# Performance work log

Measured on AMD Instinct MI355X. Metric: run time of the kernel, lower is better.

## Reference

```python
import jax, jax.numpy as jnp
import numpy as np

HIDDEN = 1024
HEADS = 16
HEAD_DIM = HIDDEN // HEADS
SCALE = HEAD_DIM ** (-0.5)


def setup_inputs() -> dict:
    key = jax.random.key(0)
    ks = jax.random.split(key, 5)
    B, N, C = 8, 1024, HIDDEN
    x = jax.random.normal(ks[0], (B, N, C), dtype=jnp.float32)
    # torch nn.Linear params: weight [out, in], bias [out]
    w_in = jax.random.normal(ks[1], (3 * C, C), dtype=jnp.float32) * (C ** -0.5)
    b_in = jax.random.normal(ks[2], (3 * C,), dtype=jnp.float32) * 0.02
    w_out = jax.random.normal(ks[3], (C, C), dtype=jnp.float32) * (C ** -0.5)
    b_out = jax.random.normal(ks[4], (C,), dtype=jnp.float32) * 0.02
    return {"x": x, "w_in": w_in, "b_in": b_in, "w_out": w_out, "b_out": b_out}


def reference(x, w_in, b_in, w_out, b_out):
    B, N, C = x.shape
    H, D = HEADS, HEAD_DIM
    # in_proj: [B,N,3C] -> (3,B,H,N,D)
    qkv = x @ w_in.T + b_in
    qkv = qkv.reshape(B, N, 3, H, D).transpose(2, 0, 3, 1, 4)
    q, k, v = qkv[0], qkv[1], qkv[2]
    # attention scores scaled after QK^T (same math as scaling q)
    attn = jnp.einsum("bhnd,bhmd->bhnm", q, k) * SCALE
    attn = jax.nn.softmax(attn, axis=-1)
    out = jnp.einsum("bhnm,bhmd->bhnd", attn, v)  # [B,H,N,D]
    out = out.transpose(0, 2, 1, 3).reshape(B, N, C)
    return out @ w_out.T + b_out
```

## Files before the change

### kernel.cpp

```cpp
#include <hip/hip_runtime.h>


typedef __attribute__((ext_vector_type(8))) __bf16 bf16x8;
typedef __attribute__((ext_vector_type(4))) __bf16 bf16x4;
typedef __attribute__((ext_vector_type(4))) float f32x4;
typedef __attribute__((ext_vector_type(4))) short short4v;

__device__ __forceinline__ f32x4 mfma16(bf16x8 a, bf16x8 b, f32x4 c) {
  return __builtin_amdgcn_mfma_f32_16x16x32_bf16(a, b, c, 0, 0, 0);
}

#if __has_builtin(__builtin_amdgcn_mfma_f32_16x16x16bf16_1k)
__device__ __forceinline__ f32x4 mfma_pv(bf16x4 a, bf16x4 b, f32x4 c) {
  short4v as = __builtin_bit_cast(short4v, a);
  short4v bs = __builtin_bit_cast(short4v, b);
  return __builtin_amdgcn_mfma_f32_16x16x16bf16_1k(as, bs, c, 0, 0, 0);
}
#else
__device__ __forceinline__ f32x4 mfma_pv(bf16x4 a, bf16x4 b, f32x4 c) {
  __bf16 z = (__bf16)0.f;
  bf16x8 a8 = {a[0], a[1], a[2], a[3], z, z, z, z};
  bf16x8 b8 = {b[0], b[1], b[2], b[3], z, z, z, z};
  return mfma16(a8, b8, c);
}
#endif

__device__ __forceinline__ float fexp2(float x) {
#if __has_builtin(__builtin_amdgcn_exp2f)
  return __builtin_amdgcn_exp2f(x);
#else
  return exp2f(x);
#endif
}

typedef __attribute__((address_space(1))) const unsigned int gu32;
typedef __attribute__((address_space(3))) unsigned int lu32;

__device__ __forceinline__ void async16(const void* g, void* l) {
  __builtin_amdgcn_global_load_lds((gu32*)g, (lu32*)l, 16, 0, 0);
}

__global__ __launch_bounds__(256) void cvt_all(const float* __restrict__ x,
                                               __bf16* __restrict__ xb,
                                               const float* __restrict__ wi,
                                               __bf16* __restrict__ wib,
                                               const float* __restrict__ wo,
                                               __bf16* __restrict__ wob) {
  int blk = blockIdx.x;
  const float* in;
  __bf16* out;
  int base;
  if (blk < 4096)      { in = x;  out = xb;  base = 0; }
  else if (blk < 5632) { in = wi; out = wib; base = 4096; }
  else                 { in = wo; out = wob; base = 5632; }
  int i = ((blk - base) * 256 + threadIdx.x) * 8;
  float4 a = *(const float4*)(in + i);
  float4 b = *(const float4*)(in + i + 4);
  bf16x8 o;
  o[0] = (__bf16)a.x; o[1] = (__bf16)a.y; o[2] = (__bf16)a.z; o[3] = (__bf16)a.w;
  o[4] = (__bf16)b.x; o[5] = (__bf16)b.y; o[6] = (__bf16)b.z; o[7] = (__bf16)b.w;
  *(bf16x8*)(out + i) = o;
}

template <bool WRITE_VT>
__global__ __launch_bounds__(512, 4) void gemm1(const __bf16* __restrict__ A,
                                                const __bf16* __restrict__ Bm,
                                                const float* __restrict__ bias,
                                                __bf16* __restrict__ C,
                                                __bf16* __restrict__ vt) {
  __shared__ char lds[49152];
  const int t = threadIdx.x;
  const int wv = t >> 6, lane = t & 63;
  const int q16 = lane & 15, quad = lane >> 4;
  const int wm = wv >> 1, wn = wv & 1;
  const int bid = blockIdx.x;
  const long m0 = (long)(bid & 31) * 256;
  const long n0 = (long)(bid >> 5) * 128;

  const int sr4 = t >> 2;
  const int gc = (t & 3) ^ ((sr4 >> 1) & 3);
  const int ldst = wv * 1024;

  const __bf16* srcA0 = A + (m0 + sr4) * 1024 + gc * 8;
  const __bf16* srcA1 = A + (m0 + 128 + sr4) * 1024 + gc * 8;
  const __bf16* srcB  = Bm + (n0 + sr4) * 1024 + gc * 8;

  const int raB = (wm * 64 + q16) * 64 + ((quad ^ ((q16 >> 1) & 3)) * 16);
  const int rbB = (wn * 64 + q16) * 64 + ((quad ^ ((q16 >> 1) & 3)) * 16);

  f32x4 zero = {0.f, 0.f, 0.f, 0.f};
  f32x4 acc[4][4];
#pragma unroll
  for (int i = 0; i < 4; ++i)
#pragma unroll
    for (int j = 0; j < 4; ++j) acc[i][j] = zero;

  async16(srcA0, lds + ldst);
  async16(srcA1, lds + 8192 + ldst);
  async16(srcB, lds + 16384 + ldst);
  __syncthreads();

  int cur = 0;
#pragma unroll 1
  for (int t32 = 0; t32 < 32; ++t32) {
    char* Ac = lds + cur * 24576;
    char* Bc = Ac + 16384;

    if (t32 < 31) {
      char* S = lds + (cur ^ 1) * 24576;
      const int kt = (t32 + 1) * 32;
      async16(srcA0 + kt, S + ldst);
      async16(srcA1 + kt, S + 8192 + ldst);
      async16(srcB + kt, S + 16384 + ldst);
    }

    bf16x8 af[4], bfr[4];
#pragma unroll
    for (int mi = 0; mi < 4; ++mi)
      af[mi] = *(const bf16x8*)(Ac + raB + mi * 1024);
#pragma unroll
    for (int nj = 0; nj < 4; ++nj)
      bfr[nj] = *(const bf16x8*)(Bc + rbB + nj * 1024);

    __builtin_amdgcn_s_setprio(1);
#pragma unroll
    for (int mi = 0; mi < 4; ++mi)
#pragma unroll
      for (int nj = 0; nj < 4; ++nj)
        acc[mi][nj] = mfma16(af[mi], bfr[nj], acc[mi][nj]);
    __builtin_amdgcn_s_setprio(0);

    __syncthreads();
    cur ^= 1;
  }

  if (WRITE_VT && n0 >= 2048) {
    const int b = (int)(m0 >> 10);
    const int nbase = (int)(m0 & 1023) + wm * 64;
#pragma unroll
    for (int nj = 0; nj < 4; ++nj) {
      int col = (int)n0 + wn * 64 + nj * 16 + q16;
      int cc = col - 2048;
      int h = cc >> 6, d = cc & 63;
      float bs = bias[col];
      __bf16* vrow = vt + (((long)(b * 16 + h)) << 16) + (long)d * 1024;
#pragma unroll
      for (int mi = 0; mi < 4; ++mi) {
        int n = nbase + mi * 16 + quad * 4;
        bf16x4 o;
#pragma unroll
        for (int r = 0; r < 4; ++r) o[r] = (__bf16)(acc[mi][nj][r] + bs);
        *(bf16x4*)(vrow + n) = o;
      }
    }
  } else {
#pragma unroll
    for (int nj = 0; nj < 4; ++nj) {
      long col = n0 + wn * 64 + nj * 16 + q16;
      float bs = bias[col];
#pragma unroll
      for (int mi = 0; mi < 4; ++mi) {
        long rowb = m0 + wm * 64 + mi * 16 + quad * 4;
#pragma unroll
        for (int r = 0; r < 4; ++r) {
          float v = acc[mi][nj][r] + bs;
          C[(rowb + r) * 3072 + col] = (__bf16)v;
        }
      }
    }
  }
}

__global__ __launch_bounds__(256, 4) void gemm2(const __bf16* __restrict__ A,
                                                const __bf16* __restrict__ Bm,
                                                const float* __restrict__ bias,
                                                float* __restrict__ C) {
  __shared__ char lds[24576];
  const int t = threadIdx.x;
  const int wv = t >> 6, lane = t & 63;
  const int q16 = lane & 15, quad = lane >> 4;
  const int wm = wv >> 1, wn = wv & 1;
  const long m0 = (long)blockIdx.x * 64;
  const long n0 = (long)blockIdx.y * 128;

  const int sr2 = t >> 2;
  const int gc = (t & 3) ^ ((sr2 >> 1) & 3);
  const int ldst = wv * 1024;

  const __bf16* srcA  = A + (m0 + sr2) * 1024 + gc * 8;
  const __bf16* srcB0 = Bm + (n0 + sr2) * 1024 + gc * 8;
  const __bf16* srcB1 = Bm + (n0 + 64 + sr2) * 1024 + gc * 8;

  const int raB = (wm * 32 + q16) * 64 + ((quad ^ ((q16 >> 1) & 3)) * 16);
  const int rbB = (wn * 64 + q16) * 64 + ((quad ^ ((q16 >> 1) & 3)) * 16);

  f32x4 zero = {0.f, 0.f, 0.f, 0.f};
  f32x4 acc[2][4];
#pragma unroll
  for (int i = 0; i < 2; ++i)
#pragma unroll
    for (int j = 0; j < 4; ++j) acc[i][j] = zero;

  async16(srcA, lds + ldst);
  async16(srcB0, lds + 4096 + ldst);
  async16(srcB1, lds + 8192 + ldst);
  __syncthreads();

  int cur = 0;
#pragma unroll 1
  for (int t32 = 0; t32 < 32; ++t32) {
    char* Ac = lds + cur * 12288;
    char* Bc = Ac + 4096;

    if (t32 < 31) {
      char* S = lds + (cur ^ 1) * 12288;
      const int kt = (t32 + 1) * 32;
      async16(srcA + kt, S + ldst);
      async16(srcB0 + kt, S + 4096 + ldst);
      async16(srcB1 + kt, S + 8192 + ldst);
    }

    bf16x8 af[2], bfr[4];
#pragma unroll
    for (int mi = 0; mi < 2; ++mi)
      af[mi] = *(const bf16x8*)(Ac + raB + mi * 1024);
#pragma unroll
    for (int nj = 0; nj < 4; ++nj)
      bfr[nj] = *(const bf16x8*)(Bc + rbB + nj * 1024);

    __builtin_amdgcn_s_setprio(1);
#pragma unroll
    for (int mi = 0; mi < 2; ++mi)
#pragma unroll
      for (int nj = 0; nj < 4; ++nj)
        acc[mi][nj] = mfma16(af[mi], bfr[nj], acc[mi][nj]);
    __builtin_amdgcn_s_setprio(0);

    __syncthreads();
    cur ^= 1;
  }

#pragma unroll
  for (int nj = 0; nj < 4; ++nj) {
    long col = n0 + wn * 64 + nj * 16 + q16;
    float bs = bias[col];
#pragma unroll
    for (int mi = 0; mi < 2; ++mi) {
      long rowb = m0 + wm * 32 + mi * 16 + quad * 4;
#pragma unroll
      for (int r = 0; r < 4; ++r) {
        float v = acc[mi][nj][r] + bs;
        C[(rowb + r) * 1024 + col] = v;
      }
    }
  }
}

__global__ __launch_bounds__(256, 4) void attn_kernel(const __bf16* __restrict__ qkv,
                                                      const __bf16* __restrict__ vt,
                                                      __bf16* __restrict__ ao) {
  __shared__ __bf16 Ks[64 * 64];
  __shared__ __bf16 Vt[64 * 64];
  const int t = threadIdx.x;
  const int wv = t >> 6, lane = t & 63;
  const int q16 = lane & 15, quad = lane >> 4;
  const int bh = blockIdx.x;
  const int b = bh >> 4, h = bh & 15;
  const int q0 = blockIdx.y * 128;
  const long rowbase = (long)b * 1024;

  bf16x8 qf0[2], qf1[2];
#pragma unroll
  for (int qh = 0; qh < 2; ++qh) {
    long qrow = rowbase + q0 + qh * 64 + wv * 16 + q16;
    const __bf16* qp = qkv + qrow * 3072 + h * 64 + quad * 8;
    bf16x8 a = *(const bf16x8*)qp;
    bf16x8 c = *(const bf16x8*)(qp + 32);
#pragma unroll
    for (int j = 0; j < 8; ++j) {
      a[j] = (__bf16)((float)a[j] * 0.18033688f);
      c[j] = (__bf16)((float)c[j] * 0.18033688f);
    }
    qf0[qh] = a;
    qf1[qh] = c;
  }

  f32x4 zero = {0.f, 0.f, 0.f, 0.f};
  f32x4 oacc[2][4];
#pragma unroll
  for (int qh = 0; qh < 2; ++qh)
#pragma unroll
    for (int dt = 0; dt < 4; ++dt) oacc[qh][dt] = zero;
  float lcol0 = 0.f, lcol1 = 0.f;

  char* KsB = (char*)Ks;
  char* VtB = (char*)Vt;
  const int sr = t >> 3;
  const int sgc = (t & 7) ^ (sr & 7);
  const int sw = q16 & 7;

  for (int kv0 = 0; kv0 < 1024; kv0 += 64) {
    __syncthreads();
    const __bf16* kg = qkv + (rowbase + kv0 + sr) * 3072 + 1024 + h * 64 + sgc * 8;
    async16(kg, KsB + wv * 1024);
    async16(kg + (long)32 * 3072, KsB + 4096 + wv * 1024);
    const __bf16* vg = vt + (long)bh * 65536 + (long)sr * 1024 + kv0 + sgc * 8;
    async16(vg, VtB + wv * 1024);
    async16(vg + (long)32 * 1024, VtB + 4096 + wv * 1024);
    __syncthreads();

    f32x4 sacc[2][4];
#pragma unroll
    for (int qh = 0; qh < 2; ++qh)
#pragma unroll
      for (int nt = 0; nt < 4; ++nt) sacc[qh][nt] = zero;
#pragma unroll
    for (int nt = 0; nt < 4; ++nt) {
      int kvr = nt * 16 + q16;
      bf16x8 kf0 = *(const bf16x8*)(KsB + kvr * 128 + ((quad ^ sw) * 16));
      bf16x8 kf1 = *(const bf16x8*)(KsB + kvr * 128 + (((4 + quad) ^ sw) * 16));
#pragma unroll
      for (int qh = 0; qh < 2; ++qh) {
        sacc[qh][nt] = mfma16(kf0, qf0[qh], sacc[qh][nt]);
        sacc[qh][nt] = mfma16(kf1, qf1[qh], sacc[qh][nt]);
      }
    }

    bf16x4 pf[2][4];
#pragma unroll
    for (int qh = 0; qh < 2; ++qh) {
      float lc = 0.f;
#pragma unroll
      for (int nt = 0; nt < 4; ++nt)
#pragma unroll
        for (int r = 0; r < 4; ++r) {
          float p = fexp2(sacc[qh][nt][r]);
          lc += p;
          pf[qh][nt][r] = (__bf16)p;
        }
      if (qh == 0) lcol0 += lc; else lcol1 += lc;
    }

#pragma unroll
    for (int nt = 0; nt < 4; ++nt) {
      int c = ((nt * 2 + (quad >> 1)) ^ sw) * 16 + (quad & 1) * 8;
#pragma unroll
      for (int dt = 0; dt < 4; ++dt) {
        bf16x4 vf = *(const bf16x4*)(VtB + (dt * 16 + q16) * 128 + c);
#pragma unroll
        for (int qh = 0; qh < 2; ++qh)
          oacc[qh][dt] = mfma_pv(pf[qh][nt], vf, oacc[qh][dt]);
      }
    }
  }

#pragma unroll
  for (int qh = 0; qh < 2; ++qh) {
    float lcol = qh == 0 ? lcol0 : lcol1;
    lcol += __shfl_xor(lcol, 16);
    lcol += __shfl_xor(lcol, 32);
    float inv = 1.0f / lcol;
#pragma unroll
    for (int r = 0; r < 4; ++r) {
      float ir = __shfl(inv, quad * 4 + r);
      long orow = rowbase + q0 + qh * 64 + wv * 16 + quad * 4 + r;
#pragma unroll
      for (int dt = 0; dt < 4; ++dt)
        ao[orow * 1024 + h * 64 + dt * 16 + q16] = (__bf16)(oacc[qh][dt][r] * ir);
    }
  }
}

extern "C" void kernel_launch(void* const* d_in, const int* in_sizes, int n_in,
                              void* d_out, int out_size, void* d_ws, size_t ws_size,
                              hipStream_t stream) {
  const float* x     = (const float*)d_in[0];
  const float* w_in  = (const float*)d_in[1];
  const float* b_in  = (const float*)d_in[2];
  const float* w_out = (const float*)d_in[3];
  const float* b_out = (const float*)d_in[4];
  float* out = (float*)d_out;

  char* ws = (char*)d_ws;
  __bf16* xb   = (__bf16*)(ws);
  __bf16* wib  = (__bf16*)(ws + 16777216);
  __bf16* wob  = (__bf16*)(ws + 23068672);
  __bf16* qkvb = (__bf16*)(ws + 25165824);
  __bf16* aob  = (__bf16*)(ws + 75497472);
  __bf16* vtg  = (__bf16*)d_out;

  cvt_all<<<6144, 256, 0, stream>>>(x, xb, w_in, wib, w_out, wob);
  gemm1<true><<<768, 512, 0, stream>>>(xb, wib, b_in, qkvb, vtg);
  attn_kernel<<<dim3(128, 8), 256, 0, stream>>>(qkvb, vtg, aob);
  gemm2<<<dim3(128, 8), 256, 0, stream>>>(aob, wob, b_out, out);
}
```

Baseline: 228.8 us.

## Enlarge out-projection GEMM tiles to 128x256 with 512 threads and BK=64

Reworks the output-projection GEMM so each block computes a 128x256 tile with 8 waves, each wave owning a 64x64 sub-tile, and each K step covering 64 elements with an 8-way XOR swizzle. The aim is more operand reuse per LDS load and half as many barrier-separated iterations. In exchange it uses 96KB of LDS and more accumulator registers, and launches only 256 blocks, which may leave compute units underused.

```diff
diff --git a/kernel.cpp b/kernel.cpp
--- a/kernel.cpp
+++ b/kernel.cpp
@@ -171,70 +171,82 @@
   }
 }
 
-__global__ __launch_bounds__(256, 4) void gemm2(const __bf16* __restrict__ A,
+__global__ __launch_bounds__(512, 2) void gemm2(const __bf16* __restrict__ A,
                                                 const __bf16* __restrict__ Bm,
                                                 const float* __restrict__ bias,
                                                 float* __restrict__ C) {
-  __shared__ char lds[24576];
+  __shared__ char lds[98304];
   const int t = threadIdx.x;
   const int wv = t >> 6, lane = t & 63;
   const int q16 = lane & 15, quad = lane >> 4;
-  const int wm = wv >> 1, wn = wv & 1;
-  const long m0 = (long)blockIdx.x * 64;
-  const long n0 = (long)blockIdx.y * 128;
-
-  const int sr2 = t >> 2;
-  const int gc = (t & 3) ^ ((sr2 >> 1) & 3);
+  const int wm = wv >> 2, wn = wv & 3;
+  const long m0 = (long)blockIdx.x * 128;
+  const long n0 = (long)blockIdx.y * 256;
+
+  const int sr = t >> 3;
+  const int gc = (t & 7) ^ (sr & 7);
   const int ldst = wv * 1024;
 
-  const __bf16* srcA  = A + (m0 + sr2) * 1024 + gc * 8;
-  const __bf16* srcB0 = Bm + (n0 + sr2) * 1024 + gc * 8;
-  const __bf16* srcB1 = Bm + (n0 + 64 + sr2) * 1024 + gc * 8;
-
-  const int raB = (wm * 32 + q16) * 64 + ((quad ^ ((q16 >> 1) & 3)) * 16);
-  const int rbB = (wn * 64 + q16) * 64 + ((quad ^ ((q16 >> 1) & 3)) * 16);
+  const __bf16* srcA0 = A + (m0 + sr) * 1024 + gc * 8;
+  const __bf16* srcA1 = A + (m0 + 64 + sr) * 1024 + gc * 8;
+  const __bf16* srcB0 = Bm + (n0 + sr) * 1024 + gc * 8;
+  const __bf16* srcB1 = Bm + (n0 + 64 + sr) * 1024 + gc * 8;
+  const __bf16* srcB2 = Bm + (n0 + 128 + sr) * 1024 + gc * 8;
+  const __bf16* srcB3 = Bm + (n0 + 192 + sr) * 1024 + gc * 8;
 
   f32x4 zero = {0.f, 0.f, 0.f, 0.f};
-  f32x4 acc[2][4];
-#pragma unroll
-  for (int i = 0; i < 2; ++i)
+  f32x4 acc[4][4];
+#pragma unroll
+  for (int i = 0; i < 4; ++i)
 #pragma unroll
     for (int j = 0; j < 4; ++j) acc[i][j] = zero;
 
-  async16(srcA, lds + ldst);
-  async16(srcB0, lds + 4096 + ldst);
-  async16(srcB1, lds + 8192 + ldst);
+  async16(srcA0, lds + ldst);
+  async16(srcA1, lds + 8192 + ldst);
+  async16(srcB0, lds + 16384 + ldst);
+  async16(srcB1, lds + 24576 + ldst);
+  async16(srcB2, lds + 32768 + ldst);
+  async16(srcB3, lds + 40960 + ldst);
   __syncthreads();
 
   int cur = 0;
 #pragma unroll 1
-  for (int t32 = 0; t32 < 32; ++t32) {
-    char* Ac = lds + cur * 12288;
-    char* Bc = Ac + 4096;
-
-    if (t32 < 31) {
-      char* S = lds + (cur ^ 1) * 12288;
-      const int kt = (t32 + 1) * 32;
-      async16(srcA + kt, S + ldst);
-      async16(srcB0 + kt, S + 4096 + ldst);
-      async16(srcB1 + kt, S + 8192 + ldst);
-    }
-
-    bf16x8 af[2], bfr[4];
-#pragma unroll
-    for (int mi = 0; mi < 2; ++mi)
-      af[mi] = *(const bf16x8*)(Ac + raB + mi * 1024);
-#pragma unroll
-    for (int nj = 0; nj < 4; ++nj)
-      bfr[nj] = *(const bf16x8*)(Bc + rbB + nj * 1024);
-
-    __builtin_amdgcn_s_setprio(1);
-#pragma unroll
-    for (int mi = 0; mi < 2; ++mi)
-#pragma unroll
-      for (int nj = 0; nj < 4; ++nj)
-        acc[mi][nj] = mfma16(af[mi], bfr[nj], acc[mi][nj]);
-    __builtin_amdgcn_s_setprio(0);
+  for (int t16 = 0; t16 < 16; ++t16) {
+    char* Ac = lds + cur * 49152;
+    char* Bc = Ac + 16384;
+
+    if (t16 < 15) {
+      char* S = lds + (cur ^ 1) * 49152;
+      const int kt = (t16 + 1) * 64;
+      async16(srcA0 + kt, S + ldst);
+      async16(srcA1 + kt, S + 8192 + ldst);
+      async16(srcB0 + kt, S + 16384 + ldst);
+      async16(srcB1 + kt, S + 24576 + ldst);
+      async16(srcB2 + kt, S + 32768 + ldst);
+      async16(srcB3 + kt, S + 40960 + ldst);
+    }
+
+#pragma unroll
+    for (int kk = 0; kk < 2; ++kk) {
+      bf16x8 af[4], bfr[4];
+#pragma unroll
+      for (int mi = 0; mi < 4; ++mi) {
+        int ra = wm * 64 + mi * 16 + q16;
+        af[mi] = *(const bf16x8*)(Ac + ra * 128 + (((kk * 4 + quad) ^ (ra & 7)) * 16));
+      }
+#pragma unroll
+      for (int nj = 0; nj < 4; ++nj) {
+        int rb = wn * 64 + nj * 16 + q16;
+        bfr[nj] = *(const bf16x8*)(Bc + rb * 128 + (((kk * 4 + quad) ^ (rb & 7)) * 16));
+      }
+      __builtin_amdgcn_s_setprio(1);
+#pragma unroll
+      for (int mi = 0; mi < 4; ++mi)
+#pragma unroll
+        for (int nj = 0; nj < 4; ++nj)
+          acc[mi][nj] = mfma16(af[mi], bfr[nj], acc[mi][nj]);
+      __builtin_amdgcn_s_setprio(0);
+    }
 
     __syncthreads();
     cur ^= 1;
@@ -245,8 +257,8 @@
     long col = n0 + wn * 64 + nj * 16 + q16;
     float bs = bias[col];
 #pragma unroll
-    for (int mi = 0; mi < 2; ++mi) {
-      long rowb = m0 + wm * 32 + mi * 16 + quad * 4;
+    for (int mi = 0; mi < 4; ++mi) {
+      long rowb = m0 + wm * 64 + mi * 16 + quad * 4;
 #pragma unroll
       for (int r = 0; r < 4; ++r) {
         float v = acc[mi][nj][r] + bs;
@@ -392,5 +404,5 @@
   cvt_all<<<6144, 256, 0, stream>>>(x, xb, w_in, wib, w_out, wob);
   gemm1<true><<<768, 512, 0, stream>>>(xb, wib, b_in, qkvb, vtg);
   attn_kernel<<<dim3(128, 8), 256, 0, stream>>>(qkvb, vtg, aob);
-  gemm2<<<dim3(128, 8), 256, 0, stream>>>(aob, wob, b_out, out);
-}
+  gemm2<<<dim3(64, 4), 512, 0, stream>>>(aob, wob, b_out, out);
+}
```

Result: faster. 221.4 us (median of 3 runs) (-3.2%).
